# Optimization experiments

Measured on AMD Instinct MI355X. Metric: run time of the kernel, lower is better.

Reference implementation:

```python
import jax, jax.numpy as jnp
import numpy as np
from jax import lax

DN = ('NCDHW', 'OIDHW', 'NCDHW')
BN_EPS = 1e-5  # eval-mode BatchNorm3d with running_mean=0, running_var=1


def conv3d(x, w, b):
    y = lax.conv_general_dilated(x, w, window_strides=(1, 1, 1),
                                 padding=[(1, 1)] * 3, dimension_numbers=DN)
    return y + b[None, :, None, None, None]


def maxpool2(x):
    return lax.reduce_window(x, -jnp.inf, lax.max,
                             (1, 1, 2, 2, 2), (1, 1, 2, 2, 2), 'VALID')


def spline_block(x, cw, cb, knots, sw, w1, w2, g, beta):
    # SplineConv3d: conv -> (BSpline3D blend with SiLU) -> BN(eval) -> maxpool
    y = conv3d(x, cw, cb)                                   # [b,c,d,h,w]
    basis = jnp.maximum(y[..., None] - knots, 0.0) ** 3     # [b,c,d,h,w,k]
    sp = jnp.einsum('bcdhwk,ck->bcdhw', basis, sw)
    out = (w1[None, :, None, None, None] * sp
           + w2[None, :, None, None, None] * (y * jax.nn.sigmoid(y)))
    scale = (g / jnp.sqrt(1.0 + BN_EPS))[None, :, None, None, None]
    return maxpool2(out * scale + beta[None, :, None, None, None])


def setup_inputs() -> dict:
    key = jax.random.key(0)
    ks = iter(jax.random.split(key, 40))
    def nrm(shape, s=1.0):
        return jax.random.normal(next(ks), shape, dtype=jnp.float32) * s
    d = {}
    d['x'] = nrm((2, 1, 64, 64, 64))
    for cin, cout, t in [(1, 32, '1'), (32, 64, '2'), (64, 128, '3')]:
        d[f'c{t}_w'] = nrm((cout, cin, 3, 3, 3), 0.1)
        d[f'c{t}_b'] = nrm((cout,), 0.01)
        d[f'c{t}_knots'] = jnp.linspace(-1.0, 1.0, 10).astype(jnp.float32)
        d[f'c{t}_sw'] = nrm((cout, 10), 0.2)
        d[f'c{t}_w1'] = nrm((cout,), 0.2)
        d[f'c{t}_w2'] = nrm((cout,), 0.2)
        d[f'bn{t}_g'] = 1.0 + nrm((cout,), 0.1)
        d[f'bn{t}_b'] = nrm((cout,), 0.1)
    d['fc1_w'] = nrm((256, 128), 0.05)
    d['fc1_b'] = nrm((256,), 0.01)
    d['fc2_w'] = nrm((2, 256), 0.05)
    d['fc2_b'] = nrm((2,), 0.01)
    return d


def reference(x,
              c1_w, c1_b, c1_knots, c1_sw, c1_w1, c1_w2, bn1_g, bn1_b,
              c2_w, c2_b, c2_knots, c2_sw, c2_w1, c2_w2, bn2_g, bn2_b,
              c3_w, c3_b, c3_knots, c3_sw, c3_w1, c3_w2, bn3_g, bn3_b,
              fc1_w, fc1_b, fc2_w, fc2_b):
    h = spline_block(x, c1_w, c1_b, c1_knots, c1_sw, c1_w1, c1_w2, bn1_g, bn1_b)
    h = spline_block(h, c2_w, c2_b, c2_knots, c2_sw, c2_w1, c2_w2, bn2_g, bn2_b)
    h = spline_block(h, c3_w, c3_b, c3_knots, c3_sw, c3_w1, c3_w2, bn3_g, bn3_b)
    h = h.mean(axis=(2, 3, 4))          # AdaptiveAvgPool3d((1,1,1)) + flatten
    h = jax.nn.relu(h @ fc1_w.T + fc1_b)  # dropout is identity in eval mode
    return h @ fc2_w.T + fc2_b
```

## Files before the change

kernel.cpp:

```cpp
#include <hip/hip_runtime.h>
#include <math.h>


#define GLOBAL_AS __attribute__((address_space(1)))
#define LDS_AS    __attribute__((address_space(3)))

static __device__ __forceinline__ void async_ld16(const float* g, float* l) {
    __builtin_amdgcn_global_load_lds((const GLOBAL_AS void*)g, (LDS_AS void*)l,
                                     16, 0, 0);
}

template <int TPB_, int CIN, int CSPLIT, int G, int PDT, int PHT, int PWT>
__global__ __launch_bounds__(TPB_, 2) void spline_block_kernel(
    const float* __restrict__ x,
    const float* __restrict__ cw,
    const float* __restrict__ cb,
    const float* __restrict__ knots,
    const float* __restrict__ sw,
    const float* __restrict__ w1,
    const float* __restrict__ w2,
    const float* __restrict__ g,
    const float* __restrict__ beta,
    const float* __restrict__ zbuf,
    float* __restrict__ out,
    int N, int Cout, int D, int H, int W,
    int ntiles, int nthw, int ntw)
{
    constexpr int SP     = PDT * PHT * PWT;
    constexpr int CPG    = CIN / CSPLIT;
    constexpr int ID     = 2 * PDT + 2;
    constexpr int IH     = 2 * PHT + 2;
    constexpr int PITCH  = 24;
    constexpr int ROWS   = ID * IH;
    constexpr int CHUNKS = ROWS * 6;
    constexpr int PHYS   = ROWS * PITCH;
    constexpr int NCH    = (CHUNKS + SP - 1) / SP;
    constexpr int BUFS   = (CPG > 1) ? 2 : 1;
    static_assert(SP * CSPLIT == TPB_, "block = CSPLIT x SP");
    static_assert(CIN % CSPLIT == 0, "cin divisible");
    static_assert(NCH <= 32, "mask fits u32");
    static_assert(CSPLIT == 1 ||
                  (CSPLIT - 1) * SP * G * 8 <= CSPLIT * BUFS * PHYS,
                  "reduction scratch fits in tile");

    __shared__ __align__(16) float tile[CSPLIT][BUFS][PHYS];
    __shared__ float  wlds[CIN * G * 28];
    __shared__ float4 stbl[G * 11];

    const int PD = D >> 1, PH = H >> 1, PW = W >> 1;
    const int groups = Cout / G;
    const int tid  = threadIdx.x;
    const int cg   = tid / SP;
    const int stid = tid % SP;

    const int bx      = blockIdx.x;
    const int tile_id = bx % ntiles;
    const int t1      = bx / ntiles;
    const int grp     = t1 % groups;
    const int n       = t1 / groups;
    const int c0      = grp * G;
    const int cinbase = cg * CPG;

    const int td  = tile_id / nthw;
    const int rem = tile_id % nthw;
    const int th_ = rem / ntw;
    const int tw_ = rem % ntw;

    for (int i = tid; i < CIN * G * 27; i += TPB_) {
        const int t  = i % 27;
        const int cgr = i / 27;
        const int gg = cgr % G;
        const int ci = cgr / G;
        wlds[cgr * 28 + t] = cw[((c0 + gg) * CIN + ci) * 27 + t];
    }
    for (int i = tid; i < G * 11; i += TPB_) {
        const int gg  = i / 11;
        const int cnt = i % 11;
        const int c   = c0 + gg;
        float A = 0.f, B3 = 0.f, C3 = 0.f, Dd = 0.f;
        for (int j = 0; j < cnt; j++) {
            const float s = sw[c * 10 + j];
            const float k = knots[j];
            A  += s;
            B3 += 3.0f * s * k;
            C3 += 3.0f * s * k * k;
            Dd += s * k * k * k;
        }
        stbl[i] = make_float4(A, B3, C3, Dd);
    }

    const int pwl = stid % PWT;
    const int phl = (stid / PWT) % PHT;
    const int pdl = stid / (PWT * PHT);

    const int pd0 = td * PDT, ph0 = th_ * PHT, pw0 = tw_ * PWT;
    const int d0 = 2 * pd0 - 1, h0 = 2 * ph0 - 1;
    const int w0 = 2 * pw0 - 1;
    const int wb = w0 & ~3;
    const int woff = w0 - wb;

    int off[NCH];
    unsigned vm = 0;
#pragma unroll
    for (int k = 0; k < NCH; k++) {
        const int chunk = stid + SP * k;
        const int row = chunk / 6, cs = chunk - row * 6;
        const int dz = row / IH, hy = row - dz * IH;
        const int dd = d0 + dz, hh = h0 + hy;
        const int wsd = wb + cs * 4;
        const bool ok = (chunk < CHUNKS) &
                        ((unsigned)dd < (unsigned)D) &
                        ((unsigned)hh < (unsigned)H) &
                        ((unsigned)wsd < (unsigned)W);
        off[k] = ok ? (dd * H + hh) * W + wsd : 0;
        vm |= (unsigned)ok << k;
    }

    const size_t chstride = (size_t)D * H * W;
    const float* xn = x + (size_t)n * CIN * chstride;

    float acc[G][8];
#pragma unroll
    for (int gg = 0; gg < G; gg++)
#pragma unroll
        for (int i = 0; i < 8; i++) acc[gg][i] = 0.0f;

    __syncthreads();

    {
        const float* xc = xn + (size_t)cinbase * chstride;
        float* dst = &tile[cg][0][0];
#pragma unroll
        for (int k = 0; k < NCH; k++) {
            const int chunk = stid + SP * k;
            if ((k + 1) * SP <= CHUNKS || chunk < CHUNKS) {
                const float* src = ((vm >> k) & 1) ? (xc + off[k]) : zbuf;
                async_ld16(src, dst + chunk * 4);
            }
        }
    }
    __syncthreads();

    int cur = 0;
#pragma unroll 1
    for (int s = 0; s < CPG; s++) {
        if (s + 1 < CPG) {
            const float* xc = xn + (size_t)(cinbase + s + 1) * chstride;
            float* dst = &tile[cg][cur ^ (BUFS - 1)][0];
#pragma unroll
            for (int k = 0; k < NCH; k++) {
                const int chunk = stid + SP * k;
                if ((k + 1) * SP <= CHUNKS || chunk < CHUNKS) {
                    const float* src = ((vm >> k) & 1) ? (xc + off[k]) : zbuf;
                    async_ld16(src, dst + chunk * 4);
                }
            }
        }

        const int ci = cinbase + s;
        const float* tb = &tile[cg][cur][0];
        float r[64];
#pragma unroll
        for (int dz = 0; dz < 4; dz++)
#pragma unroll
        for (int dy = 0; dy < 4; dy++) {
            const int rb = ((2 * pdl + dz) * IH + (2 * phl + dy)) * PITCH +
                           woff + 2 * pwl;
            r[(dz * 4 + dy) * 4 + 0] = tb[rb + 0];
            r[(dz * 4 + dy) * 4 + 1] = tb[rb + 1];
            r[(dz * 4 + dy) * 4 + 2] = tb[rb + 2];
            r[(dz * 4 + dy) * 4 + 3] = tb[rb + 3];
        }

#pragma unroll
        for (int gg = 0; gg < G; gg++) {
            const float4* w4p = (const float4*)&wlds[(ci * G + gg) * 28];
#pragma unroll
            for (int ch = 0; ch < 7; ch++) {
                const float4 wv = w4p[ch];
#pragma unroll
                for (int j = 0; j < 4; j++) {
                    const int tap = ch * 4 + j;
                    if (tap < 27) {
                        const float wvj = (j == 0) ? wv.x : (j == 1) ? wv.y
                                        : (j == 2) ? wv.z : wv.w;
                        const int kd = tap / 9, kh = (tap % 9) / 3, kw = tap % 3;
#pragma unroll
                        for (int od = 0; od < 2; od++)
#pragma unroll
                        for (int oh = 0; oh < 2; oh++)
#pragma unroll
                        for (int ow = 0; ow < 2; ow++)
                            acc[gg][(od * 2 + oh) * 2 + ow] =
                                fmaf(wvj,
                                     r[((od + kd) * 4 + (oh + kh)) * 4 + (ow + kw)],
                                     acc[gg][(od * 2 + oh) * 2 + ow]);
                    }
                }
            }
        }

        if (s + 1 < CPG) {
            __syncthreads();
            cur ^= 1;
        }
    }

    float* af = &acc[0][0];
    if (CSPLIT > 1) {
        __syncthreads();
        float* scratch = &tile[0][0][0];
        if (cg > 0) {
#pragma unroll
            for (int idx = 0; idx < G * 8; idx++)
                scratch[(idx * (CSPLIT - 1) + (cg - 1)) * SP + stid] = af[idx];
        }
        __syncthreads();
        if (cg == 0) {
#pragma unroll
            for (int idx = 0; idx < G * 8; idx++) {
                float s = af[idx];
                for (int j = 0; j < CSPLIT - 1; j++)
                    s += scratch[(idx * (CSPLIT - 1) + j) * SP + stid];
                af[idx] = s;
            }
        }
    }

    if (cg == 0) {
        const int pdg = pd0 + pdl, phg = ph0 + phl, pwg = pw0 + pwl;
#pragma unroll
        for (int gg = 0; gg < G; gg++) {
            const int c = c0 + gg;
            const float bias = cb[c];
            const float W1 = w1[c], W2 = w2[c];
            const float scale = g[c] * rsqrtf(1.0f + 1e-5f);
            const float bb = beta[c];

            float m = -INFINITY;
#pragma unroll
            for (int i = 0; i < 8; i++) {
                const float y = acc[gg][i] + bias;
                int idx = (int)floorf((y + 1.0f) * 4.5f) + 1;
                idx = min(max(idx, 0), 10);
                const float4 cf = stbl[gg * 11 + idx];
                const float sp = ((cf.x * y - cf.y) * y + cf.z) * y - cf.w;
                const float silu = y / (1.0f + __expf(-y));
                const float o = fmaf(W1 * sp + W2 * silu, scale, bb);
                m = fmaxf(m, o);
            }
            out[((size_t)(n * Cout + c) * PD + pdg) * PH * PW + phg * PW + pwg] = m;
        }
    }
}

__global__ __launch_bounds__(64) void mean_kernel(
    const float* __restrict__ h, float* __restrict__ out, int S)
{
    const int nc = blockIdx.x;
    const int lane = threadIdx.x;
    const float* p = h + (size_t)nc * S;
    float s = 0.0f;
    for (int i = lane; i < S; i += 64) s += p[i];
#pragma unroll
    for (int off = 32; off > 0; off >>= 1) s += __shfl_down(s, off, 64);
    if (lane == 0) out[nc] = s / (float)S;
}

__global__ __launch_bounds__(256) void fc_kernel(
    const float* __restrict__ pooled,
    const float* __restrict__ w1, const float* __restrict__ b1,
    const float* __restrict__ w2, const float* __restrict__ b2,
    float* __restrict__ out)
{
    __shared__ float hbuf[2][256];
    const int j = threadIdx.x;
#pragma unroll
    for (int nn = 0; nn < 2; nn++) {
        float s = b1[j];
        for (int k = 0; k < 128; k++)
            s = fmaf(pooled[nn * 128 + k], w1[j * 128 + k], s);
        hbuf[nn][j] = fmaxf(s, 0.0f);
    }
    __syncthreads();
    const int wid = j >> 6, lane = j & 63;
    const int nn = wid >> 1, oo = wid & 1;
    float s = 0.0f;
    for (int k = lane; k < 256; k += 64) s += hbuf[nn][k] * w2[oo * 256 + k];
#pragma unroll
    for (int off = 32; off > 0; off >>= 1) s += __shfl_down(s, off, 64);
    if (lane == 0) out[nn * 2 + oo] = s + b2[oo];
}

extern "C" void kernel_launch(void* const* d_in, const int* in_sizes, int n_in,
                              void* d_out, int out_size, void* d_ws, size_t ws_size,
                              hipStream_t stream) {
    const float* x      = (const float*)d_in[0];
    const float* c1_w   = (const float*)d_in[1];
    const float* c1_b   = (const float*)d_in[2];
    const float* c1_kn  = (const float*)d_in[3];
    const float* c1_sw  = (const float*)d_in[4];
    const float* c1_w1  = (const float*)d_in[5];
    const float* c1_w2  = (const float*)d_in[6];
    const float* bn1_g  = (const float*)d_in[7];
    const float* bn1_b  = (const float*)d_in[8];
    const float* c2_w   = (const float*)d_in[9];
    const float* c2_b   = (const float*)d_in[10];
    const float* c2_kn  = (const float*)d_in[11];
    const float* c2_sw  = (const float*)d_in[12];
    const float* c2_w1  = (const float*)d_in[13];
    const float* c2_w2  = (const float*)d_in[14];
    const float* bn2_g  = (const float*)d_in[15];
    const float* bn2_b  = (const float*)d_in[16];
    const float* c3_w   = (const float*)d_in[17];
    const float* c3_b   = (const float*)d_in[18];
    const float* c3_kn  = (const float*)d_in[19];
    const float* c3_sw  = (const float*)d_in[20];
    const float* c3_w1  = (const float*)d_in[21];
    const float* c3_w2  = (const float*)d_in[22];
    const float* bn3_g  = (const float*)d_in[23];
    const float* bn3_b  = (const float*)d_in[24];
    const float* fc1_w  = (const float*)d_in[25];
    const float* fc1_b  = (const float*)d_in[26];
    const float* fc2_w  = (const float*)d_in[27];
    const float* fc2_b  = (const float*)d_in[28];

    float* ws = (float*)d_ws;
    float* h1     = ws;
    float* h2     = h1 + 2097152;
    float* h3     = h2 + 524288;
    float* pooled = h3 + 131072;
    float* zbuf   = pooled + 256;

    hipMemsetAsync(zbuf, 0, 64, stream);

    spline_block_kernel<256, 1, 1, 4, 4, 8, 8><<<dim3(2048), dim3(256), 0, stream>>>(
        x, c1_w, c1_b, c1_kn, c1_sw, c1_w1, c1_w2, bn1_g, bn1_b, zbuf, h1,
        2, 32, 64, 64, 64, 128, 16, 4);
    spline_block_kernel<256, 32, 1, 4, 4, 8, 8><<<dim3(512), dim3(256), 0, stream>>>(
        h1, c2_w, c2_b, c2_kn, c2_sw, c2_w1, c2_w2, bn2_g, bn2_b, zbuf, h2,
        2, 64, 32, 32, 32, 16, 4, 2);
    spline_block_kernel<256, 64, 4, 4, 2, 4, 8><<<dim3(512), dim3(256), 0, stream>>>(
        h2, c3_w, c3_b, c3_kn, c3_sw, c3_w1, c3_w2, bn3_g, bn3_b, zbuf, h3,
        2, 128, 16, 16, 16, 8, 2, 1);
    mean_kernel<<<dim3(256), dim3(64), 0, stream>>>(h3, pooled, 512);
    fc_kernel<<<dim3(1), dim3(256), 0, stream>>>(pooled, fc1_w, fc1_b, fc2_w, fc2_b,
                                                 (float*)d_out);
}
```

Baseline: 341.6 us.

## Give each wave a private input tile and replace block barriers with vmcnt waits

Splits each block's spatial tile into per-wave 2x4x8 sub-tiles, so each wave stages its own halo region into a private LDS buffer. The per-channel __syncthreads double-buffer handshake becomes an s_waitcnt vmcnt on the wave's own async global-to-LDS loads. The goal is to remove block-wide barrier stalls in the cin loop of layers 2 and 3. In exchange, the per-wave halos overlap and add redundant loads and LDS use. Correctness also depends on the hard-coded vmcnt(6) matching exactly six loads per stage and on LDS writes from global_load_lds being visible once vmcnt is satisfied.

```diff
diff --git a/kernel.cpp b/kernel.cpp
--- a/kernel.cpp
+++ b/kernel.cpp
@@ -10,7 +10,8 @@
                                      16, 0, 0);
 }
 
-template <int TPB_, int CIN, int CSPLIT, int G, int PDT, int PHT, int PWT>
+template <int TPB_, int CIN, int CSPLIT, int G,
+          int WDT, int WHT, int WWT, int BD, int BH, int BW>
 __global__ __launch_bounds__(TPB_, 2) void spline_block_kernel(
     const float* __restrict__ x,
     const float* __restrict__ cw,
@@ -26,32 +27,38 @@
     int N, int Cout, int D, int H, int W,
     int ntiles, int nthw, int ntw)
 {
-    constexpr int SP     = PDT * PHT * PWT;
+    constexpr int NSW    = BD * BH * BW;
+    constexpr int NW     = TPB_ / 64;
     constexpr int CPG    = CIN / CSPLIT;
-    constexpr int ID     = 2 * PDT + 2;
-    constexpr int IH     = 2 * PHT + 2;
-    constexpr int PITCH  = 24;
+    constexpr int ID     = 2 * WDT + 2;
+    constexpr int IH     = 2 * WHT + 2;
+    constexpr int CHK    = (WWT + 4) / 2;
+    constexpr int PITCH  = CHK * 4;
     constexpr int ROWS   = ID * IH;
-    constexpr int CHUNKS = ROWS * 6;
-    constexpr int PHYS   = ROWS * PITCH;
-    constexpr int NCH    = (CHUNKS + SP - 1) / SP;
+    constexpr int CHUNKS = ROWS * CHK;
+    constexpr int PHYS   = CHUNKS * 4;
+    constexpr int NCH    = (CHUNKS + 63) / 64;
     constexpr int BUFS   = (CPG > 1) ? 2 : 1;
-    static_assert(SP * CSPLIT == TPB_, "block = CSPLIT x SP");
+    static_assert(NW == NSW * CSPLIT, "waves = spatial-tiles x cin-split");
+    static_assert(WDT * WHT * WWT == 64, "one wave per spatial tile");
     static_assert(CIN % CSPLIT == 0, "cin divisible");
     static_assert(NCH <= 32, "mask fits u32");
+    static_assert(NCH == 6, "s_waitcnt vmcnt(6) literal assumes 6 issues/cin");
     static_assert(CSPLIT == 1 ||
-                  (CSPLIT - 1) * SP * G * 8 <= CSPLIT * BUFS * PHYS,
+                  (CSPLIT - 1) * 64 * G * 8 <= NW * BUFS * PHYS,
                   "reduction scratch fits in tile");
 
-    __shared__ __align__(16) float tile[CSPLIT][BUFS][PHYS];
+    __shared__ __align__(16) float tile[NW][BUFS][PHYS];
     __shared__ float  wlds[CIN * G * 28];
     __shared__ float4 stbl[G * 11];
 
     const int PD = D >> 1, PH = H >> 1, PW = W >> 1;
     const int groups = Cout / G;
     const int tid  = threadIdx.x;
-    const int cg   = tid / SP;
-    const int stid = tid % SP;
+    const int wv   = tid >> 6;
+    const int lane = tid & 63;
+    const int sw_  = wv % NSW;
+    const int cg   = wv / NSW;
 
     const int bx      = blockIdx.x;
     const int tile_id = bx % ntiles;
@@ -89,11 +96,18 @@
         stbl[i] = make_float4(A, B3, C3, Dd);
     }
 
-    const int pwl = stid % PWT;
-    const int phl = (stid / PWT) % PHT;
-    const int pdl = stid / (PWT * PHT);
-
-    const int pd0 = td * PDT, ph0 = th_ * PHT, pw0 = tw_ * PWT;
+    const int swd = sw_ / (BH * BW);
+    const int r2  = sw_ % (BH * BW);
+    const int swh = r2 / BW;
+    const int sww = r2 % BW;
+    const int pd0 = td  * (BD * WDT) + swd * WDT;
+    const int ph0 = th_ * (BH * WHT) + swh * WHT;
+    const int pw0 = tw_ * (BW * WWT) + sww * WWT;
+
+    const int pwl = lane % WWT;
+    const int phl = (lane / WWT) % WHT;
+    const int pdl = lane / (WWT * WHT);
+
     const int d0 = 2 * pd0 - 1, h0 = 2 * ph0 - 1;
     const int w0 = 2 * pw0 - 1;
     const int wb = w0 & ~3;
@@ -103,8 +117,8 @@
     unsigned vm = 0;
 #pragma unroll
     for (int k = 0; k < NCH; k++) {
-        const int chunk = stid + SP * k;
-        const int row = chunk / 6, cs = chunk - row * 6;
+        const int chunk = lane + 64 * k;
+        const int row = chunk / CHK, cs = chunk - row * CHK;
         const int dz = row / IH, hy = row - dz * IH;
         const int dd = d0 + dz, hh = h0 + hy;
         const int wsd = wb + cs * 4;
@@ -127,38 +141,33 @@
 
     __syncthreads();
 
-    {
-        const float* xc = xn + (size_t)cinbase * chstride;
-        float* dst = &tile[cg][0][0];
+    auto stage = [&](int ci, int buf) {
+        const float* xc = xn + (size_t)ci * chstride;
+        float* dst = &tile[wv][buf][0];
 #pragma unroll
         for (int k = 0; k < NCH; k++) {
-            const int chunk = stid + SP * k;
-            if ((k + 1) * SP <= CHUNKS || chunk < CHUNKS) {
+            const int chunk = lane + 64 * k;
+            if ((k + 1) * 64 <= CHUNKS || chunk < CHUNKS) {
                 const float* src = ((vm >> k) & 1) ? (xc + off[k]) : zbuf;
                 async_ld16(src, dst + chunk * 4);
             }
         }
-    }
-    __syncthreads();
-
-    int cur = 0;
+    };
+
+    stage(cinbase, 0);
+
 #pragma unroll 1
     for (int s = 0; s < CPG; s++) {
+        const int cur = s & (BUFS - 1);
         if (s + 1 < CPG) {
-            const float* xc = xn + (size_t)(cinbase + s + 1) * chstride;
-            float* dst = &tile[cg][cur ^ (BUFS - 1)][0];
-#pragma unroll
-            for (int k = 0; k < NCH; k++) {
-                const int chunk = stid + SP * k;
-                if ((k + 1) * SP <= CHUNKS || chunk < CHUNKS) {
-                    const float* src = ((vm >> k) & 1) ? (xc + off[k]) : zbuf;
-                    async_ld16(src, dst + chunk * 4);
-                }
-            }
+            stage(cinbase + s + 1, cur ^ 1);
+            asm volatile("s_waitcnt vmcnt(6)" ::: "memory");
+        } else {
+            asm volatile("s_waitcnt vmcnt(0)" ::: "memory");
         }
 
         const int ci = cinbase + s;
-        const float* tb = &tile[cg][cur][0];
+        const float* tb = &tile[wv][cur][0];
         float r[64];
 #pragma unroll
         for (int dz = 0; dz < 4; dz++)
@@ -177,13 +186,13 @@
             const float4* w4p = (const float4*)&wlds[(ci * G + gg) * 28];
 #pragma unroll
             for (int ch = 0; ch < 7; ch++) {
-                const float4 wv = w4p[ch];
+                const float4 wv4 = w4p[ch];
 #pragma unroll
                 for (int j = 0; j < 4; j++) {
                     const int tap = ch * 4 + j;
                     if (tap < 27) {
-                        const float wvj = (j == 0) ? wv.x : (j == 1) ? wv.y
-                                        : (j == 2) ? wv.z : wv.w;
+                        const float wvj = (j == 0) ? wv4.x : (j == 1) ? wv4.y
+                                        : (j == 2) ? wv4.z : wv4.w;
                         const int kd = tap / 9, kh = (tap % 9) / 3, kw = tap % 3;
 #pragma unroll
                         for (int od = 0; od < 2; od++)
@@ -199,11 +208,6 @@
                 }
             }
         }
-
-        if (s + 1 < CPG) {
-            __syncthreads();
-            cur ^= 1;
-        }
     }
 
     float* af = &acc[0][0];
@@ -213,16 +217,16 @@
         if (cg > 0) {
 #pragma unroll
             for (int idx = 0; idx < G * 8; idx++)
-                scratch[(idx * (CSPLIT - 1) + (cg - 1)) * SP + stid] = af[idx];
+                scratch[(idx * (CSPLIT - 1) + (cg - 1)) * 64 + lane] = af[idx];
         }
         __syncthreads();
         if (cg == 0) {
 #pragma unroll
             for (int idx = 0; idx < G * 8; idx++) {
-                float s = af[idx];
+                float s2 = af[idx];
                 for (int j = 0; j < CSPLIT - 1; j++)
-                    s += scratch[(idx * (CSPLIT - 1) + j) * SP + stid];
-                af[idx] = s;
+                    s2 += scratch[(idx * (CSPLIT - 1) + j) * 64 + lane];
+                af[idx] = s2;
             }
         }
     }
@@ -334,13 +338,16 @@
 
     hipMemsetAsync(zbuf, 0, 64, stream);
 
-    spline_block_kernel<256, 1, 1, 4, 4, 8, 8><<<dim3(2048), dim3(256), 0, stream>>>(
+    spline_block_kernel<256, 1, 1, 4, 2, 4, 8, 2, 2, 1>
+        <<<dim3(2048), dim3(256), 0, stream>>>(
         x, c1_w, c1_b, c1_kn, c1_sw, c1_w1, c1_w2, bn1_g, bn1_b, zbuf, h1,
         2, 32, 64, 64, 64, 128, 16, 4);
-    spline_block_kernel<256, 32, 1, 4, 4, 8, 8><<<dim3(512), dim3(256), 0, stream>>>(
+    spline_block_kernel<256, 32, 1, 4, 2, 4, 8, 2, 2, 1>
+        <<<dim3(512), dim3(256), 0, stream>>>(
         h1, c2_w, c2_b, c2_kn, c2_sw, c2_w1, c2_w2, bn2_g, bn2_b, zbuf, h2,
         2, 64, 32, 32, 32, 16, 4, 2);
-    spline_block_kernel<256, 64, 4, 4, 2, 4, 8><<<dim3(512), dim3(256), 0, stream>>>(
+    spline_block_kernel<256, 64, 4, 4, 2, 4, 8, 1, 1, 1>
+        <<<dim3(512), dim3(256), 0, stream>>>(
         h2, c3_w, c3_b, c3_kn, c3_sw, c3_w1, c3_w2, bn3_g, bn3_b, zbuf, h3,
         2, 128, 16, 16, 16, 8, 2, 1);
     mean_kernel<<<dim3(256), dim3(64), 0, stream>>>(h3, pooled, 512);
```

Measured after the change: 324.8 us. 1.05x faster.
